# Kernel optimization log

Measured on AMD Instinct MI355X. Metric: run time of the kernel, lower is better.

Reference implementation:

```python
import jax, jax.numpy as jnp
import numpy as np

H = 2048        # hidden_size
NH = 16         # num query heads
NKV = 4         # num kv heads
HD = H // NH    # head_dim = 128
G = NH // NKV   # kv groups = 4
EPS = 1e-12


def setup_inputs() -> dict:
    key = jax.random.key(0)
    ks = jax.random.split(key, 20)
    B, S = 2, 2048
    s = 1.0 / np.sqrt(H)
    inp = {
        "hidden_states": jax.random.normal(ks[0], (B, S, H), jnp.float32),
        "source_states": jax.random.normal(ks[1], (B, S, H), jnp.float32),
        # weights stored [in, out] so y = x @ W + b
        "Wq": jax.random.normal(ks[2], (H, NH * HD), jnp.float32) * s,
        "bq": jnp.zeros((NH * HD,), jnp.float32),
        "Wk": jax.random.normal(ks[3], (H, NKV * HD), jnp.float32) * s,
        "bk": jnp.zeros((NKV * HD,), jnp.float32),
        "Wv": jax.random.normal(ks[4], (H, NKV * HD), jnp.float32) * s,
        "bv": jnp.zeros((NKV * HD,), jnp.float32),
        "Wd": jax.random.normal(ks[5], (H, H), jnp.float32) * s,
        "bd": jnp.zeros((H,), jnp.float32),
        "W1": jax.random.normal(ks[6], (H, H), jnp.float32) * s,
        "b1": jnp.zeros((H,), jnp.float32),
        "W2": jax.random.normal(ks[7], (H, H), jnp.float32) * s,
        "b2": jnp.zeros((H,), jnp.float32),
        "gamma": jnp.ones((H,), jnp.float32),
        "beta": jnp.zeros((H,), jnp.float32),
    }
    return inp


def _layernorm(x, gamma, beta):
    mu = jnp.mean(x, axis=-1, keepdims=True)
    var = jnp.mean(jnp.square(x - mu), axis=-1, keepdims=True)
    return (x - mu) * jax.lax.rsqrt(var + EPS) * gamma + beta


def reference(hidden_states, source_states, Wq, bq, Wk, bk, Wv, bv, Wd, bd,
              W1, b1, W2, b2, gamma, beta):
    B, Sq, _ = hidden_states.shape
    Ss = source_states.shape[1]
    # FFN-gate on source: Pl1 = relu(lin1(src)); P = lin2(Pl1) + Pl1
    Pl1 = jax.nn.relu(source_states @ W1 + b1)
    P = (Pl1 @ W2 + b2) + Pl1
    # projections; K/V grouped into NKV heads, Q into NH = NKV*G heads
    K = (P @ Wk + bk).reshape(B, Ss, NKV, HD).transpose(0, 2, 1, 3)        # b k s d
    V = (P @ Wv + bv).reshape(B, Ss, NKV, HD).transpose(0, 2, 1, 3)        # b k s d
    Q = (hidden_states @ Wq + bq).reshape(B, Sq, NKV, G, HD)
    Q = Q.transpose(0, 2, 3, 1, 4)                                          # b k g q d
    scores = jnp.einsum('bkgqd,bksd->bkgqs', Q, K) / np.sqrt(HD)
    probs = jax.nn.softmax(scores, axis=-1)
    ctx = jnp.einsum('bkgqs,bksd->bkgqd', probs, V)                         # b k g q d
    ctx = ctx.transpose(0, 3, 1, 2, 4).reshape(B, Sq, NH * HD)              # b q h*d
    out = ctx @ Wd + bd
    return _layernorm(out + hidden_states, gamma, beta)
```

## Files before the change

### kernel.cpp

```cpp
#include <hip/hip_runtime.h>
#include <hip/hip_bf16.h>

typedef __bf16 bf16;
typedef __bf16 bf16x2 __attribute__((ext_vector_type(2)));
typedef __bf16 bf16x4 __attribute__((ext_vector_type(4)));
typedef __bf16 bf16x8 __attribute__((ext_vector_type(8)));
typedef float  f32x4  __attribute__((ext_vector_type(4)));
typedef unsigned int u32x4 __attribute__((ext_vector_type(4)));

#define H_   2048
#define S_   2048
#define B_   2
#define NH_  16
#define NKV_ 4
#define HD_  128
#define KVS  1024

#define QSCALE 0.12751743f

__device__ __forceinline__ f32x4 mfma16(bf16x8 a, bf16x8 b, f32x4 c) {
  return __builtin_amdgcn_mfma_f32_16x16x32_bf16(a, b, c, 0, 0, 0);
}

typedef __attribute__((address_space(3))) unsigned int lds_u32_t;
typedef const __attribute__((address_space(1))) unsigned int glb_u32_t;
__device__ __forceinline__ void glds16(const bf16* g, bf16* l) {
  __builtin_amdgcn_global_load_lds((glb_u32_t*)g, (lds_u32_t*)l, 16, 0, 0);
}

__device__ __forceinline__ unsigned pk2(float a, float b) {
  bf16x2 v = { (bf16)a, (bf16)b };
  return __builtin_bit_cast(unsigned, v);
}

__global__ __launch_bounds__(256)
void prep(const float* __restrict__ Wq, const float* __restrict__ W1,
          const float* __restrict__ W2, const float* __restrict__ Wd,
          const float* __restrict__ Wk, const float* __restrict__ Wv,
          const float* __restrict__ hidden, const float* __restrict__ source,
          bf16* __restrict__ Wqt, bf16* __restrict__ W1t,
          bf16* __restrict__ W2t, bf16* __restrict__ Wdt,
          bf16* __restrict__ Wkt, bf16* __restrict__ Wvt,
          bf16* __restrict__ hb,  bf16* __restrict__ sb)
{
  __shared__ bf16 t[32][33];
  int idx = blockIdx.x;
  if (idx < 16384) {
    const float* in = (idx < 8192) ? hidden : source;
    bf16*       out = (idx < 8192) ? hb : sb;
    const int i = idx & 8191;
    const size_t off = ((size_t)i * 256 + threadIdx.x) * 4;
    const float4 v = *(const float4*)(in + off);
    bf16x4 o = { (bf16)v.x, (bf16)v.y, (bf16)v.z, (bf16)v.w };
    *(bf16x4*)(out + off) = o;
    return;
  }
  idx -= 16384;
  const float* in; bf16* out; int N;
  if      (idx < 4096)  { in = Wq; out = Wqt; N = 2048; }
  else if (idx < 8192)  { in = W1; out = W1t; N = 2048; idx -= 4096; }
  else if (idx < 12288) { in = W2; out = W2t; N = 2048; idx -= 8192; }
  else if (idx < 16384) { in = Wd; out = Wdt; N = 2048; idx -= 12288; }
  else if (idx < 17408) { in = Wk; out = Wkt; N = 512;  idx -= 16384; }
  else                  { in = Wv; out = Wvt; N = 512;  idx -= 17408; }
  const int K = 2048;
  const int tx = threadIdx.x & 31, ty = threadIdx.x >> 5;
  const int k0 = (idx & 63) * 32, n0 = (idx >> 6) * 32;
  #pragma unroll
  for (int i = 0; i < 4; i++)
    t[ty + i*8][tx] = (bf16)in[(size_t)(k0 + ty + i*8) * N + n0 + tx];
  __syncthreads();
  #pragma unroll
  for (int i = 0; i < 4; i++)
    out[(size_t)(n0 + ty + i*8) * K + k0 + tx] = t[tx][ty + i*8];
}

__global__ __launch_bounds__(256)
void transpose_v(const bf16* __restrict__ KVin, bf16* __restrict__ Vt)
{
  __shared__ bf16 t[32][33];
  const int tx = threadIdx.x & 31, ty = threadIdx.x >> 5;
  const int s0 = blockIdx.x * 32, d0 = blockIdx.y * 32;
  const int bk = blockIdx.z;
  const int b = bk >> 2, kv = bk & 3;
  const bf16* src = KVin + (size_t)b * S_ * KVS + 512 + kv * HD_;
  #pragma unroll
  for (int i = 0; i < 4; i++)
    t[ty + i*8][tx] = src[(size_t)(s0 + ty + i*8) * KVS + d0 + tx];
  __syncthreads();
  bf16* dst = Vt + (size_t)bk * HD_ * S_;
  #pragma unroll
  for (int i = 0; i < 4; i++)
    dst[(size_t)(d0 + ty + i*8) * S_ + s0 + tx] = t[tx][ty + i*8];
}

__device__ __forceinline__
void gemm_body(const bf16* __restrict__ A, const bf16* __restrict__ Wt,
               const float* __restrict__ bias, const float* __restrict__ bias2,
               int nsplit, const bf16* __restrict__ resid,
               bf16* __restrict__ outB, int N, int K, int relu, float oscale,
               int m0, int n0, bf16* As, bf16* Bs)
{
  const int tid  = threadIdx.x;
  const int lane = tid & 63;
  const int w    = tid >> 6;
  const int wm = w & 1, wn = w >> 1;
  const int quad = lane >> 4, l16 = lane & 15;
  const int g_r = lane >> 2;
  const int g_c = (lane & 3) * 8;

  const f32x4 fz = {0.f, 0.f, 0.f, 0.f};
  f32x4 acc[4][4];
  #pragma unroll
  for (int i = 0; i < 4; i++)
    #pragma unroll
    for (int j = 0; j < 4; j++) acc[i][j] = fz;

  auto stage = [&](int nb, int k0) {
    #pragma unroll
    for (int i = 0; i < 2; i++) {
      const int rb = (w*2 + i) * 16;
      glds16(A  + (size_t)(m0 + rb + g_r) * K + k0 + g_c, As + nb*4096 + rb*32 + lane*8);
      glds16(Wt + (size_t)(n0 + rb + g_r) * K + k0 + g_c, Bs + nb*4096 + rb*32 + lane*8);
    }
  };

  stage(0, 0);
  const int NK = K >> 5;
  for (int it = 0; it < NK; it++) {
    const int bf = it & 1;
    __syncthreads();
    if (it + 1 < NK) stage(bf ^ 1, (it + 1) << 5);
    bf16x8 af[4], bfr[4];
    #pragma unroll
    for (int i = 0; i < 4; i++)
      af[i]  = *(const bf16x8*)(As + bf*4096 + (wm*64 + i*16 + l16)*32 + quad*8);
    #pragma unroll
    for (int j = 0; j < 4; j++)
      bfr[j] = *(const bf16x8*)(Bs + bf*4096 + (wn*64 + j*16 + l16)*32 + quad*8);
    #pragma unroll
    for (int i = 0; i < 4; i++)
      #pragma unroll
      for (int j = 0; j < 4; j++)
        acc[i][j] = mfma16(af[i], bfr[j], acc[i][j]);
  }

  #pragma unroll
  for (int i = 0; i < 4; i++) {
    const int row = m0 + wm*64 + i*16 + quad*4;
    #pragma unroll
    for (int j = 0; j < 4; j++) {
      const int col = n0 + wn*64 + j*16 + l16;
      const float bi = (col < nsplit) ? bias[col] : bias2[col - nsplit];
      #pragma unroll
      for (int r = 0; r < 4; r++) {
        float v = acc[i][j][r] + bi;
        if (relu) v = fmaxf(v, 0.f);
        v *= oscale;
        size_t idx = (size_t)(row + r) * N + col;
        if (resid) v += (float)resid[idx];
        outB[idx] = (bf16)v;
      }
    }
  }
}

__global__ __launch_bounds__(256)
void gemm_one(const bf16* __restrict__ A, const bf16* __restrict__ Wt,
              const float* __restrict__ bias, const float* __restrict__ bias2,
              int nsplit, const bf16* __restrict__ resid,
              bf16* __restrict__ outB, int N, int K, int relu, float oscale)
{
  __shared__ __align__(16) bf16 As[2*128*32];
  __shared__ __align__(16) bf16 Bs[2*128*32];
  gemm_body(A, Wt, bias, bias2, nsplit, resid, outB, N, K, relu, oscale,
            blockIdx.y*128, blockIdx.x*128, As, Bs);
}

__global__ __launch_bounds__(256)
void gemm_dual(const bf16* __restrict__ A0, const bf16* __restrict__ W0,
               const float* __restrict__ b0, bf16* __restrict__ o0,
               int relu0, float s0,
               const bf16* __restrict__ A1, const bf16* __restrict__ W1,
               const float* __restrict__ b1, bf16* __restrict__ o1,
               int relu1, float s1, int N, int K)
{
  __shared__ __align__(16) bf16 As[2*128*32];
  __shared__ __align__(16) bf16 Bs[2*128*32];
  if (blockIdx.z == 0)
    gemm_body(A0, W0, b0, b0, 1<<30, nullptr, o0, N, K, relu0, s0,
              blockIdx.y*128, blockIdx.x*128, As, Bs);
  else
    gemm_body(A1, W1, b1, b1, 1<<30, nullptr, o1, N, K, relu1, s1,
              blockIdx.y*128, blockIdx.x*128, As, Bs);
}

__global__ __launch_bounds__(256)
void attn_partial(const bf16* __restrict__ Q, const bf16* __restrict__ KV,
                  const bf16* __restrict__ Vt, bf16* __restrict__ OpBase,
                  float* __restrict__ LsBase)
{
  __shared__ __align__(16) bf16 Ks[2*4096];
  __shared__ __align__(16) bf16 Vs[2*4096];
  const int tid = threadIdx.x;
  const int lane = tid & 63, w = tid >> 6;
  const int quad = lane >> 4, l16 = lane & 15;
  const int qt = blockIdx.x, h = blockIdx.y;
  const int b = blockIdx.z >> 1, sh = blockIdx.z & 1;
  const int kv = h >> 2;
  const int qbase = qt * 128 + w * 32;
  const int s_begin = sh * (S_/2);

  bf16*  Op = OpBase + (size_t)sh * 8388608;
  float* Lp = LsBase + (size_t)sh * (B_*NH_*S_);

  const bf16* Qp = Q  + ((size_t)b * S_ + qbase) * H_ + h * HD_;
  const bf16* Kp = KV + (size_t)b * S_ * KVS + kv * HD_;
  const bf16* Vp = Vt + (size_t)(b * NKV_ + kv) * HD_ * S_;

  const int fr = lane & 15;
  const int fc = (lane >> 4) * 8;

  const f32x4 fz = {0.f, 0.f, 0.f, 0.f};

  bf16x8 qf[2][4];
  #pragma unroll
  for (int i = 0; i < 2; i++)
    #pragma unroll
    for (int kt = 0; kt < 4; kt++)
      qf[i][kt] = *(const bf16x8*)(Qp + (size_t)(i*16 + l16) * H_ + kt*32 + quad*8);

  f32x4 o[2][8];
  #pragma unroll
  for (int i = 0; i < 2; i++)
    #pragma unroll
    for (int n = 0; n < 8; n++) o[i][n] = fz;
  float lsum[2] = {0.f, 0.f};

  auto stageKV = [&](int nb, int s0) {
    bf16* Kb = Ks + nb*4096;
    bf16* Vb = Vs + nb*4096;
    glds16(Kp + (size_t)(s0 +      fr) * KVS + w*32 + fc, Kb + (w*2+0)*512 + lane*8);
    glds16(Kp + (size_t)(s0 + 16 + fr) * KVS + w*32 + fc, Kb + (w*2+1)*512 + lane*8);
    glds16(Vp + (size_t)(w*16     + fr) * S_ + s0 + fc,   Vb + w*512       + lane*8);
    glds16(Vp + (size_t)((4+w)*16 + fr) * S_ + s0 + fc,   Vb + (4+w)*512   + lane*8);
  };

  stageKV(0, s_begin);

  const int NIT = (S_/2) / 32;
  for (int it = 0; it < NIT; it++) {
    const int bf = it & 1;
    __syncthreads();
    if (it + 1 < NIT) stageKV(bf ^ 1, s_begin + (it + 1) * 32);

    const bf16* Kb = Ks + bf*4096;
    f32x4 sa[2][2];
    sa[0][0] = fz; sa[0][1] = fz; sa[1][0] = fz; sa[1][1] = fz;
    __builtin_amdgcn_s_setprio(1);
    #pragma unroll
    for (int kt = 0; kt < 4; kt++) {
      bf16x8 kf0 = *(const bf16x8*)(Kb + (kt*2+0)*512 + lane*8);
      bf16x8 kf1 = *(const bf16x8*)(Kb + (kt*2+1)*512 + lane*8);
      #pragma unroll
      for (int i = 0; i < 2; i++) {
        sa[i][0] = mfma16(kf0, qf[i][kt], sa[i][0]);
        sa[i][1] = mfma16(kf1, qf[i][kt], sa[i][1]);
      }
    }
    __builtin_amdgcn_s_setprio(0);

    bf16x8 pf[2];
    #pragma unroll
    for (int i = 0; i < 2; i++) {
      float p[2][4];
      #pragma unroll
      for (int nt = 0; nt < 2; nt++)
        #pragma unroll
        for (int r = 0; r < 4; r++) {
          p[nt][r] = exp2f(sa[i][nt][r]);
          lsum[i] += p[nt][r];
        }
      unsigned Apk = pk2(p[0][0], p[0][1]);
      unsigned Bpk = pk2(p[0][2], p[0][3]);
      unsigned Cpk = pk2(p[1][0], p[1][1]);
      unsigned Dpk = pk2(p[1][2], p[1][3]);
      const int srcL = l16 + ((quad & 1) << 5);
      const bool hi = (quad >= 2);
      const unsigned a0 = __shfl(Apk, srcL),      b0 = __shfl(Bpk, srcL);
      const unsigned a1 = __shfl(Apk, srcL + 16), b1 = __shfl(Bpk, srcL + 16);
      const unsigned c0 = __shfl(Cpk, srcL),      d0 = __shfl(Dpk, srcL);
      const unsigned c1 = __shfl(Cpk, srcL + 16), d1 = __shfl(Dpk, srcL + 16);
      u32x4 t;
      t.x = hi ? c0 : a0;
      t.y = hi ? d0 : b0;
      t.z = hi ? c1 : a1;
      t.w = hi ? d1 : b1;
      pf[i] = __builtin_bit_cast(bf16x8, t);
    }

    const bf16* Vb = Vs + bf*4096;
    __builtin_amdgcn_s_setprio(1);
    #pragma unroll
    for (int nt = 0; nt < 8; nt++) {
      bf16x8 vf = *(const bf16x8*)(Vb + nt*512 + lane*8);
      o[0][nt] = mfma16(pf[0], vf, o[0][nt]);
      o[1][nt] = mfma16(pf[1], vf, o[1][nt]);
    }
    __builtin_amdgcn_s_setprio(0);
  }

  bf16* op = Op + ((size_t)b * S_ + qbase) * H_ + h * HD_;
  #pragma unroll
  for (int i = 0; i < 2; i++)
    #pragma unroll
    for (int nt = 0; nt < 8; nt++)
      #pragma unroll
      for (int r = 0; r < 4; r++)
        op[(size_t)(i*16 + quad*4 + r) * H_ + nt*16 + l16] = (bf16)o[i][nt][r];

  float* lp = Lp + (size_t)(b * NH_ + h) * S_ + qbase;
  #pragma unroll
  for (int i = 0; i < 2; i++) {
    float s = lsum[i];
    s += __shfl_xor(s, 16);
    s += __shfl_xor(s, 32);
    if (lane < 16) lp[i*16 + lane] = s;
  }
}

__global__ __launch_bounds__(256)
void attn_combine(const bf16* __restrict__ O0, const bf16* __restrict__ O1,
                  const float* __restrict__ L0, const float* __restrict__ L1,
                  bf16* __restrict__ ctx)
{
  const int row = blockIdx.x;
  const int b = row >> 11, s = row & 2047;
  const int tid = threadIdx.x;
  const int h = tid >> 4;
  const size_t idx = (size_t)row * H_ + tid * 8;
  const size_t li  = (size_t)(b * NH_ + h) * S_ + s;
  const float rinv = 1.f / (L0[li] + L1[li]);
  bf16x8 a = *(const bf16x8*)(O0 + idx);
  bf16x8 c = *(const bf16x8*)(O1 + idx);
  bf16x8 o;
  #pragma unroll
  for (int k = 0; k < 8; k++)
    o[k] = (bf16)(((float)a[k] + (float)c[k]) * rinv);
  *(bf16x8*)(ctx + idx) = o;
}

__global__ __launch_bounds__(256)
void ln_fused(const bf16* __restrict__ a, const float* __restrict__ hidden,
              const float* __restrict__ gamma, const float* __restrict__ beta,
              float* __restrict__ out)
{
  __shared__ float red[8];
  const int row = blockIdx.x;
  const bf16*  pa = a      + (size_t)row * H_;
  const float* pb = hidden + (size_t)row * H_;
  float x[8]; float s = 0.f, s2 = 0.f;
  #pragma unroll
  for (int j = 0; j < 8; j++) {
    int c = threadIdx.x + j*256;
    float v = (float)pa[c] + pb[c];
    x[j] = v; s += v; s2 += v*v;
  }
  #pragma unroll
  for (int off = 1; off < 64; off <<= 1) {
    s  += __shfl_xor(s,  off);
    s2 += __shfl_xor(s2, off);
  }
  const int wv = threadIdx.x >> 6;
  if ((threadIdx.x & 63) == 0) { red[wv] = s; red[4 + wv] = s2; }
  __syncthreads();
  s  = red[0] + red[1] + red[2] + red[3];
  s2 = red[4] + red[5] + red[6] + red[7];
  const float mu   = s * (1.0f / H_);
  const float var  = s2 * (1.0f / H_) - mu * mu;
  const float rstd = rsqrtf(var + 1e-12f);
  float* po = out + (size_t)row * H_;
  #pragma unroll
  for (int j = 0; j < 8; j++) {
    int c = threadIdx.x + j*256;
    po[c] = ((x[j] - mu) * rstd) * gamma[c] + beta[c];
  }
}

extern "C" void kernel_launch(void* const* d_in, const int* in_sizes, int n_in,
                              void* d_out, int out_size, void* d_ws, size_t ws_size,
                              hipStream_t stream)
{
  (void)in_sizes; (void)n_in; (void)out_size; (void)ws_size;
  const float* hidden = (const float*)d_in[0];
  const float* source = (const float*)d_in[1];
  const float* Wq = (const float*)d_in[2];
  const float* bq = (const float*)d_in[3];
  const float* Wk = (const float*)d_in[4];
  const float* bk = (const float*)d_in[5];
  const float* Wv = (const float*)d_in[6];
  const float* bv = (const float*)d_in[7];
  const float* Wd = (const float*)d_in[8];
  const float* bd = (const float*)d_in[9];
  const float* W1 = (const float*)d_in[10];
  const float* b1 = (const float*)d_in[11];
  const float* W2 = (const float*)d_in[12];
  const float* b2 = (const float*)d_in[13];
  const float* gamma = (const float*)d_in[14];
  const float* beta  = (const float*)d_in[15];

  char* ws = (char*)d_ws;
  const size_t M = 1048576;
  bf16*  rHB = (bf16*)(ws + 0*M);
  bf16*  rSB = (bf16*)(ws + 16*M);
  bf16*  Qb  = (bf16*)(ws + 32*M);
  bf16*  Wqt = (bf16*)(ws + 48*M);
  bf16*  W2t = (bf16*)(ws + 56*M);
  bf16*  W1t = (bf16*)(ws + 64*M);
  bf16*  Wdt = (bf16*)(ws + 72*M);
  bf16*  Wkt = (bf16*)(ws + 80*M);
  bf16*  Wvt = (bf16*)(ws + 82*M);
  bf16*  Pl1 = (bf16*)(ws + 84*M);
  bf16*  KVb = (bf16*)(ws + 84*M);
  bf16*  Vtb = (bf16*)(ws + 92*M);
  float* Ls  = (float*)(ws + 48*M);
  bf16*  Pb  = rHB;
  bf16*  O0  = rHB;
  bf16*  O1  = rSB;
  bf16*  ctx = (bf16*)(ws + 56*M);
  bf16*  oFb = Qb;

  prep<<<34816, 256, 0, stream>>>(Wq, W1, W2, Wd, Wk, Wv, hidden, source,
                                  Wqt, W1t, W2t, Wdt, Wkt, Wvt, rHB, rSB);
  gemm_dual<<<dim3(16,32,2), 256, 0, stream>>>(
      rHB, Wqt, bq, Qb,  0, QSCALE,
      rSB, W1t, b1, Pl1, 1, 1.0f, 2048, 2048);
  gemm_one<<<dim3(16,32), 256, 0, stream>>>(Pl1, W2t, b2, b2, 1<<30, Pl1,
                                            Pb, 2048, 2048, 0, 1.0f);
  gemm_one<<<dim3(8,32), 256, 0, stream>>>(Pb, Wkt, bk, bv, 512, nullptr,
                                           KVb, 1024, 2048, 0, 1.0f);
  transpose_v<<<dim3(64,4,8), 256, 0, stream>>>(KVb, Vtb);
  attn_partial<<<dim3(16,16,4), 256, 0, stream>>>(Qb, KVb, Vtb, O0, Ls);
  attn_combine<<<4096, 256, 0, stream>>>(O0, O1, Ls, Ls + B_*NH_*S_, ctx);
  gemm_one<<<dim3(16,32), 256, 0, stream>>>(ctx, Wdt, bd, bd, 1<<30, nullptr,
                                            oFb, 2048, 2048, 0, 1.0f);
  ln_fused<<<4096, 256, 0, stream>>>(oFb, hidden, gamma, beta, (float*)d_out);
}
```

Before: 599.1 us.

## Write Q/K/V in MFMA fragment-tiled layout and triple-buffer attention loads

The Q and K/V projection GEMM epilogues now scatter their outputs straight into a tiled layout that matches the attention kernel's MFMA fragments. This removes the separate V transpose kernel and lets attention stage contiguous 4KB tiles. The attention loop moves from double to triple buffering, with an explicit vmcnt wait and a raw s_barrier in place of __syncthreads, so loads run further ahead of compute. The cost is scattered, uncoalesced bf16 stores in the GEMM epilogues and more LDS per block, which may lower occupancy.

```diff
diff --git a/kernel.cpp b/kernel.cpp
--- a/kernel.cpp
+++ b/kernel.cpp
@@ -32,6 +32,7 @@
   bf16x2 v = { (bf16)a, (bf16)b };
   return __builtin_bit_cast(unsigned, v);
 }
+
 
 __global__ __launch_bounds__(256)
 void prep(const float* __restrict__ Wq, const float* __restrict__ W1,
@@ -75,30 +76,12 @@
     out[(size_t)(n0 + ty + i*8) * K + k0 + tx] = t[tx][ty + i*8];
 }
 
-__global__ __launch_bounds__(256)
-void transpose_v(const bf16* __restrict__ KVin, bf16* __restrict__ Vt)
-{
-  __shared__ bf16 t[32][33];
-  const int tx = threadIdx.x & 31, ty = threadIdx.x >> 5;
-  const int s0 = blockIdx.x * 32, d0 = blockIdx.y * 32;
-  const int bk = blockIdx.z;
-  const int b = bk >> 2, kv = bk & 3;
-  const bf16* src = KVin + (size_t)b * S_ * KVS + 512 + kv * HD_;
-  #pragma unroll
-  for (int i = 0; i < 4; i++)
-    t[ty + i*8][tx] = src[(size_t)(s0 + ty + i*8) * KVS + d0 + tx];
-  __syncthreads();
-  bf16* dst = Vt + (size_t)bk * HD_ * S_;
-  #pragma unroll
-  for (int i = 0; i < 4; i++)
-    dst[(size_t)(d0 + ty + i*8) * S_ + s0 + tx] = t[tx][ty + i*8];
-}
-
 __device__ __forceinline__
 void gemm_body(const bf16* __restrict__ A, const bf16* __restrict__ Wt,
                const float* __restrict__ bias, const float* __restrict__ bias2,
                int nsplit, const bf16* __restrict__ resid,
-               bf16* __restrict__ outB, int N, int K, int relu, float oscale,
+               bf16* __restrict__ outB, bf16* __restrict__ outC,
+               int N, int K, int relu, float oscale, int mode,
                int m0, int n0, bf16* As, bf16* Bs)
 {
   const int tid  = threadIdx.x;
@@ -157,9 +140,34 @@
         float v = acc[i][j][r] + bi;
         if (relu) v = fmaxf(v, 0.f);
         v *= oscale;
-        size_t idx = (size_t)(row + r) * N + col;
-        if (resid) v += (float)resid[idx];
-        outB[idx] = (bf16)v;
+        const int rowg = row + r;
+        if (mode == 0) {
+          size_t idx = (size_t)rowg * N + col;
+          if (resid) v += (float)resid[idx];
+          outB[idx] = (bf16)v;
+        } else if (mode == 1) {
+          const int bb = rowg >> 11, s = rowg & 2047;
+          if (col < 512) {
+            const int kvq = col >> 7, d = col & 127;
+            size_t off = ((size_t)((bb*4 + kvq)*64 + (s >> 5))) * 4096
+                       + ((d >> 5)*2 + ((s >> 4) & 1)) * 512
+                       + (((d >> 3) & 3)*16 + (s & 15)) * 8 + (d & 7);
+            outB[off] = (bf16)v;
+          } else {
+            const int kvq = (col - 512) >> 7, d = (col - 512) & 127;
+            size_t off = ((size_t)((bb*4 + kvq)*64 + (s >> 5))) * 4096
+                       + (d >> 4) * 512
+                       + (((s & 31) >> 3)*16 + (d & 15)) * 8 + (s & 7);
+            outC[off] = (bf16)v;
+          }
+        } else {
+          const int bb = rowg >> 11, q = rowg & 2047;
+          const int hh = col >> 7, d = col & 127;
+          size_t off = ((size_t)((bb*16 + hh)*64 + (q >> 5))) * 4096
+                     + ((d >> 5)*2 + ((q >> 4) & 1)) * 512
+                     + (((d >> 3) & 3)*16 + (q & 15)) * 8 + (d & 7);
+          outB[off] = (bf16)v;
+        }
       }
     }
   }
@@ -169,12 +177,13 @@
 void gemm_one(const bf16* __restrict__ A, const bf16* __restrict__ Wt,
               const float* __restrict__ bias, const float* __restrict__ bias2,
               int nsplit, const bf16* __restrict__ resid,
-              bf16* __restrict__ outB, int N, int K, int relu, float oscale)
+              bf16* __restrict__ outB, bf16* __restrict__ outC,
+              int N, int K, int relu, float oscale, int mode)
 {
   __shared__ __align__(16) bf16 As[2*128*32];
   __shared__ __align__(16) bf16 Bs[2*128*32];
-  gemm_body(A, Wt, bias, bias2, nsplit, resid, outB, N, K, relu, oscale,
-            blockIdx.y*128, blockIdx.x*128, As, Bs);
+  gemm_body(A, Wt, bias, bias2, nsplit, resid, outB, outC, N, K, relu, oscale,
+            mode, blockIdx.y*128, blockIdx.x*128, As, Bs);
 }
 
 __global__ __launch_bounds__(256)
@@ -188,20 +197,20 @@
   __shared__ __align__(16) bf16 As[2*128*32];
   __shared__ __align__(16) bf16 Bs[2*128*32];
   if (blockIdx.z == 0)
-    gemm_body(A0, W0, b0, b0, 1<<30, nullptr, o0, N, K, relu0, s0,
-              blockIdx.y*128, blockIdx.x*128, As, Bs);
+    gemm_body(A0, W0, b0, b0, 1<<30, nullptr, o0, nullptr, N, K, relu0, s0,
+              2 , blockIdx.y*128, blockIdx.x*128, As, Bs);
   else
-    gemm_body(A1, W1, b1, b1, 1<<30, nullptr, o1, N, K, relu1, s1,
-              blockIdx.y*128, blockIdx.x*128, As, Bs);
-}
-
-__global__ __launch_bounds__(256)
-void attn_partial(const bf16* __restrict__ Q, const bf16* __restrict__ KV,
-                  const bf16* __restrict__ Vt, bf16* __restrict__ OpBase,
+    gemm_body(A1, W1, b1, b1, 1<<30, nullptr, o1, nullptr, N, K, relu1, s1,
+              0, blockIdx.y*128, blockIdx.x*128, As, Bs);
+}
+
+__global__ __launch_bounds__(256)
+void attn_partial(const bf16* __restrict__ QF, const bf16* __restrict__ KF,
+                  const bf16* __restrict__ VF, bf16* __restrict__ OpBase,
                   float* __restrict__ LsBase)
 {
-  __shared__ __align__(16) bf16 Ks[2*4096];
-  __shared__ __align__(16) bf16 Vs[2*4096];
+  __shared__ __align__(16) bf16 Ks[3*4096];
+  __shared__ __align__(16) bf16 Vs[3*4096];
   const int tid = threadIdx.x;
   const int lane = tid & 63, w = tid >> 6;
   const int quad = lane >> 4, l16 = lane & 15;
@@ -209,17 +218,13 @@
   const int b = blockIdx.z >> 1, sh = blockIdx.z & 1;
   const int kv = h >> 2;
   const int qbase = qt * 128 + w * 32;
-  const int s_begin = sh * (S_/2);
 
   bf16*  Op = OpBase + (size_t)sh * 8388608;
   float* Lp = LsBase + (size_t)sh * (B_*NH_*S_);
 
-  const bf16* Qp = Q  + ((size_t)b * S_ + qbase) * H_ + h * HD_;
-  const bf16* Kp = KV + (size_t)b * S_ * KVS + kv * HD_;
-  const bf16* Vp = Vt + (size_t)(b * NKV_ + kv) * HD_ * S_;
-
-  const int fr = lane & 15;
-  const int fc = (lane >> 4) * 8;
+  const bf16* Ktile = KF + ((size_t)((b*4 + kv) * 64)) * 4096;
+  const bf16* Vtile = VF + ((size_t)((b*4 + kv) * 64)) * 4096;
+  const bf16* Qt    = QF + ((size_t)((b*16 + h) * 64 + (qbase >> 5))) * 4096;
 
   const f32x4 fz = {0.f, 0.f, 0.f, 0.f};
 
@@ -228,7 +233,7 @@
   for (int i = 0; i < 2; i++)
     #pragma unroll
     for (int kt = 0; kt < 4; kt++)
-      qf[i][kt] = *(const bf16x8*)(Qp + (size_t)(i*16 + l16) * H_ + kt*32 + quad*8);
+      qf[i][kt] = *(const bf16x8*)(Qt + (kt*2 + i)*512 + lane*8);
 
   f32x4 o[2][8];
   #pragma unroll
@@ -237,24 +242,36 @@
     for (int n = 0; n < 8; n++) o[i][n] = fz;
   float lsum[2] = {0.f, 0.f};
 
-  auto stageKV = [&](int nb, int s0) {
+  auto stageKV = [&](int nb, int t5) {
+    const bf16* kt_ = Ktile + (size_t)t5 * 4096;
+    const bf16* vt_ = Vtile + (size_t)t5 * 4096;
     bf16* Kb = Ks + nb*4096;
     bf16* Vb = Vs + nb*4096;
-    glds16(Kp + (size_t)(s0 +      fr) * KVS + w*32 + fc, Kb + (w*2+0)*512 + lane*8);
-    glds16(Kp + (size_t)(s0 + 16 + fr) * KVS + w*32 + fc, Kb + (w*2+1)*512 + lane*8);
-    glds16(Vp + (size_t)(w*16     + fr) * S_ + s0 + fc,   Vb + w*512       + lane*8);
-    glds16(Vp + (size_t)((4+w)*16 + fr) * S_ + s0 + fc,   Vb + (4+w)*512   + lane*8);
+    glds16(kt_ + (w*2+0)*512 + lane*8, Kb + (w*2+0)*512 + lane*8);
+    glds16(kt_ + (w*2+1)*512 + lane*8, Kb + (w*2+1)*512 + lane*8);
+    glds16(vt_ + (w    )*512 + lane*8, Vb + (w    )*512 + lane*8);
+    glds16(vt_ + (4+w  )*512 + lane*8, Vb + (4+w  )*512 + lane*8);
   };
 
-  stageKV(0, s_begin);
-
-  const int NIT = (S_/2) / 32;
+  const int t5b = sh * 32;
+  stageKV(0, t5b);
+  stageKV(1, t5b + 1);
+
+  const int NIT = 32;
+  int cur = 0;
   for (int it = 0; it < NIT; it++) {
-    const int bf = it & 1;
-    __syncthreads();
-    if (it + 1 < NIT) stageKV(bf ^ 1, s_begin + (it + 1) * 32);
-
-    const bf16* Kb = Ks + bf*4096;
+    if (it < NIT - 1) { asm volatile("s_waitcnt vmcnt(4)" ::: "memory"); }
+    else              { asm volatile("s_waitcnt vmcnt(0)" ::: "memory"); }
+    __builtin_amdgcn_sched_barrier(0);
+    __builtin_amdgcn_s_barrier();
+    __builtin_amdgcn_sched_barrier(0);
+    if (it + 2 < NIT) {
+      int pre = cur + 2; if (pre >= 3) pre -= 3;
+      stageKV(pre, t5b + it + 2);
+    }
+
+    const bf16* Kb = Ks + cur*4096;
+    const bf16* Vb = Vs + cur*4096;
     f32x4 sa[2][2];
     sa[0][0] = fz; sa[0][1] = fz; sa[1][0] = fz; sa[1][1] = fz;
     __builtin_amdgcn_s_setprio(1);
@@ -299,7 +316,6 @@
       pf[i] = __builtin_bit_cast(bf16x8, t);
     }
 
-    const bf16* Vb = Vs + bf*4096;
     __builtin_amdgcn_s_setprio(1);
     #pragma unroll
     for (int nt = 0; nt < 8; nt++) {
@@ -308,6 +324,8 @@
       o[1][nt] = mfma16(pf[1], vf, o[1][nt]);
     }
     __builtin_amdgcn_s_setprio(0);
+
+    cur = (cur == 2) ? 0 : cur + 1;
   }
 
   bf16* op = Op + ((size_t)b * S_ + qbase) * H_ + h * HD_;
@@ -413,7 +431,7 @@
   const size_t M = 1048576;
   bf16*  rHB = (bf16*)(ws + 0*M);
   bf16*  rSB = (bf16*)(ws + 16*M);
-  bf16*  Qb  = (bf16*)(ws + 32*M);
+  bf16*  QF  = (bf16*)(ws + 32*M);
   bf16*  Wqt = (bf16*)(ws + 48*M);
   bf16*  W2t = (bf16*)(ws + 56*M);
   bf16*  W1t = (bf16*)(ws + 64*M);
@@ -421,28 +439,26 @@
   bf16*  Wkt = (bf16*)(ws + 80*M);
   bf16*  Wvt = (bf16*)(ws + 82*M);
   bf16*  Pl1 = (bf16*)(ws + 84*M);
-  bf16*  KVb = (bf16*)(ws + 84*M);
-  bf16*  Vtb = (bf16*)(ws + 92*M);
+  bf16*  KF  = (bf16*)(ws + 84*M);
+  bf16*  VF  = (bf16*)(ws + 88*M);
   float* Ls  = (float*)(ws + 48*M);
   bf16*  Pb  = rHB;
   bf16*  O0  = rHB;
-  bf16*  O1  = rSB;
   bf16*  ctx = (bf16*)(ws + 56*M);
-  bf16*  oFb = Qb;
+  bf16*  oFb = QF;
 
   prep<<<34816, 256, 0, stream>>>(Wq, W1, W2, Wd, Wk, Wv, hidden, source,
                                   Wqt, W1t, W2t, Wdt, Wkt, Wvt, rHB, rSB);
   gemm_dual<<<dim3(16,32,2), 256, 0, stream>>>(
-      rHB, Wqt, bq, Qb,  0, QSCALE,
+      rHB, Wqt, bq, QF,  0, QSCALE,
       rSB, W1t, b1, Pl1, 1, 1.0f, 2048, 2048);
   gemm_one<<<dim3(16,32), 256, 0, stream>>>(Pl1, W2t, b2, b2, 1<<30, Pl1,
-                                            Pb, 2048, 2048, 0, 1.0f);
+                                            Pb, nullptr, 2048, 2048, 0, 1.0f, 0);
   gemm_one<<<dim3(8,32), 256, 0, stream>>>(Pb, Wkt, bk, bv, 512, nullptr,
-                                           KVb, 1024, 2048, 0, 1.0f);
-  transpose_v<<<dim3(64,4,8), 256, 0, stream>>>(KVb, Vtb);
-  attn_partial<<<dim3(16,16,4), 256, 0, stream>>>(Qb, KVb, Vtb, O0, Ls);
-  attn_combine<<<4096, 256, 0, stream>>>(O0, O1, Ls, Ls + B_*NH_*S_, ctx);
+                                           KF, VF, 1024, 2048, 0, 1.0f, 1);
+  attn_partial<<<dim3(16,16,4), 256, 0, stream>>>(QF, KF, VF, O0, Ls);
+  attn_combine<<<4096, 256, 0, stream>>>(O0, rSB, Ls, Ls + B_*NH_*S_, ctx);
   gemm_one<<<dim3(16,32), 256, 0, stream>>>(ctx, Wdt, bd, bd, 1<<30, nullptr,
-                                            oFb, 2048, 2048, 0, 1.0f);
+                                            oFb, nullptr, 2048, 2048, 0, 1.0f, 0);
   ln_fused<<<4096, 256, 0, stream>>>(oFb, hidden, gamma, beta, (float*)d_out);
 }
```

After: 597.4 us. No clear change (-0.3%).
